# Performance work log

Measured on AMD Instinct MI355X. Metric: run time of the kernel, lower is better.

Reference implementation:

```python
import jax, jax.numpy as jnp
import numpy as np

N = 50000
E = 800000
NODE_IN, EDGE_IN, HID, OUT, L = 32, 16, 128, 128, 2


def _layer_norm(h, g, b, eps=1e-5):
    mu = jnp.mean(h, axis=-1, keepdims=True)
    var = jnp.var(h, axis=-1, keepdims=True)
    return (h - mu) * jax.lax.rsqrt(var + eps) * g + b


def setup_inputs() -> dict:
    key = jax.random.key(0)
    ks = jax.random.split(key, 20)
    s = lambda k, shape, fan: jax.random.normal(k, shape, jnp.float32) * (1.0 / np.sqrt(fan))
    return {
        "x": jax.random.normal(ks[0], (N, NODE_IN), jnp.float32),
        "edge_index": jax.random.randint(ks[1], (2, E), 0, N, jnp.int64),
        "edge_attr": jax.random.normal(ks[2], (E, EDGE_IN), jnp.float32),
        "enc_W": s(ks[3], (NODE_IN, HID), NODE_IN),
        "enc_b": jnp.zeros((HID,), jnp.float32),
        "enc_g": jnp.ones((HID,), jnp.float32),
        "enc_beta": jnp.zeros((HID,), jnp.float32),
        "msg_W1": s(ks[4], (L, 2 * HID + EDGE_IN, HID), 2 * HID + EDGE_IN),
        "msg_b1": jnp.zeros((L, HID), jnp.float32),
        "msg_W2": s(ks[5], (L, HID, HID), HID),
        "msg_b2": jnp.zeros((L, HID), jnp.float32),
        "upd_W1": s(ks[6], (L, 2 * HID, HID), 2 * HID),
        "upd_b1": jnp.zeros((L, HID), jnp.float32),
        "upd_W2": s(ks[7], (L, HID, HID), HID),
        "upd_b2": jnp.zeros((L, HID), jnp.float32),
        "ln_g": jnp.ones((L, HID), jnp.float32),
        "ln_beta": jnp.zeros((L, HID), jnp.float32),
        "head_W": s(ks[8], (HID, OUT), HID),
        "head_b": jnp.zeros((OUT,), jnp.float32),
    }


def reference(x, edge_index, edge_attr, enc_W, enc_b, enc_g, enc_beta,
              msg_W1, msg_b1, msg_W2, msg_b2, upd_W1, upd_b1, upd_W2, upd_b2,
              ln_g, ln_beta, head_W, head_b):
    src = edge_index[0]  # x_j (source)
    tgt = edge_index[1]  # x_i (target, aggregation index)
    n = x.shape[0]

    # node encoder: Linear -> ReLU -> LayerNorm
    h = jax.nn.relu(x @ enc_W + enc_b)
    h = _layer_norm(h, enc_g, enc_beta)

    # per-edge incoming-degree for mean aggregation (isolated nodes -> 0)
    cnt = jax.ops.segment_sum(jnp.ones((tgt.shape[0],), h.dtype), tgt, num_segments=n)
    denom = jnp.maximum(cnt, 1.0)[:, None]

    for l in range(L):
        x_i = h[tgt]                                 # [E, HID]
        x_j = h[src]                                 # [E, HID]
        msg_in = jnp.concatenate([x_i, x_j, edge_attr], axis=-1)  # [E, 2H+Ed]
        m = jax.nn.relu(msg_in @ msg_W1[l] + msg_b1[l]) @ msg_W2[l] + msg_b2[l]
        aggr = jax.ops.segment_sum(m, tgt, num_segments=n) / denom  # mean
        upd_in = jnp.concatenate([h, aggr], axis=-1)
        out = jax.nn.relu(upd_in @ upd_W1[l] + upd_b1[l]) @ upd_W2[l] + upd_b2[l]
        h = _layer_norm(h + out, ln_g[l], ln_beta[l])

    return h @ head_W + head_b
```

## Files before the change

### kernel.cpp

```cpp
#include <hip/hip_runtime.h>
#include <hip/hip_bf16.h>
#include <stdint.h>

#define N_NODES 50000
#define N_EDGES 800000
#define NL 2

#define KS2 136
#define KSU 264
#define ESTR 132

typedef __bf16 bf16x8 __attribute__((ext_vector_type(8)));
typedef float f32x4 __attribute__((ext_vector_type(4)));

__device__ __forceinline__ f32x4 mfma_bf16(uint4 a, uint4 b, f32x4 c) {
    return __builtin_amdgcn_mfma_f32_16x16x32_bf16(
        __builtin_bit_cast(bf16x8, a), __builtin_bit_cast(bf16x8, b), c, 0, 0, 0);
}

__device__ __forceinline__ unsigned short f2b(float f) {
    union { float f; unsigned u; } v; v.f = f;
    unsigned r = v.u + 0x7FFFu + ((v.u >> 16) & 1u);
    return (unsigned short)(r >> 16);
}

__device__ __forceinline__ float b2f(unsigned short u) {
    union { unsigned u; float f; } v; v.u = ((unsigned)u) << 16; return v.f;
}
__device__ __forceinline__ float b2f_lo(unsigned u) {
    union { unsigned u; float f; } v; v.u = u << 16; return v.f;
}
__device__ __forceinline__ float b2f_hi(unsigned u) {
    union { unsigned u; float f; } v; v.u = u & 0xFFFF0000u; return v.f;
}

template<int KSTEPS, int BSTR>
__device__ __forceinline__ void gemm8(const unsigned short* aLane,
                                      const unsigned short* bLane, f32x4 acc[8]) {
#pragma unroll
    for (int kc = 0; kc < KSTEPS; kc++) {
        uint4 a = *(const uint4*)(aLane + kc * 32);
#pragma unroll
        for (int ct = 0; ct < 8; ct++) {
            uint4 b = *(const uint4*)(bLane + (size_t)ct * 16 * BSTR + kc * 32);
            acc[ct] = mfma_bf16(a, b, acc[ct]);
        }
    }
}

template<int KSTEPS, int ASTR, int BSTR>
__device__ __forceinline__ void gemm_2x4(const unsigned short* aLane,
                                         const unsigned short* bLane,
                                         f32x4 acc[4][2]) {
#pragma unroll
    for (int kc = 0; kc < KSTEPS; kc++) {
        uint4 b0 = *(const uint4*)(bLane + kc * 32);
        uint4 b1 = *(const uint4*)(bLane + (size_t)16 * BSTR + kc * 32);
#pragma unroll
        for (int rt = 0; rt < 4; rt++) {
            uint4 a = *(const uint4*)(aLane + (size_t)rt * 16 * ASTR + kc * 32);
            acc[rt][0] = mfma_bf16(a, b0, acc[rt][0]);
            acc[rt][1] = mfma_bf16(a, b1, acc[rt][1]);
        }
    }
}

__global__ void prep_kernel(const float* __restrict__ mW1,
                            const float* __restrict__ uW1, const float* __restrict__ uW2,
                            const float* __restrict__ hW,
                            unsigned short* __restrict__ wab, unsigned short* __restrict__ w1cp,
                            unsigned short* __restrict__ u1t, unsigned short* __restrict__ u2t,
                            unsigned short* __restrict__ ht) {
    int i = blockIdx.x * 256 + threadIdx.x;
    const int SA = NL * 256 * 136;
    const int SC = NL * 128 * 32;
    const int SU = NL * 128 * KSU;
    const int S3 = NL * 128 * KS2;
    const int S4 = 128 * KS2;
    if (i < SA) {
        int l = i / (256 * 136), r = i % (256 * 136), j = r / 136, k = r % 136;
        float v = 0.f;
        if (k < 128)
            v = (j < 128) ? mW1[((size_t)l * 272 + k) * 128 + j]
                          : mW1[((size_t)l * 272 + 128 + k) * 128 + (j - 128)];
        wab[i] = f2b(v);
        return;
    }
    i -= SA;
    if (i < SC) {
        int l = i / (128 * 32), r = i % (128 * 32), j = r / 32, k = r % 32;
        w1cp[i] = (k < 16) ? f2b(mW1[((size_t)l * 272 + 256 + k) * 128 + j]) : (unsigned short)0;
        return;
    }
    i -= SC;
    if (i < SU) {
        int l = i / (128 * KSU), r = i % (128 * KSU), n = r / KSU, k = r % KSU;
        if (k < 128)       u1t[i] = f2b(uW1[((size_t)l * 256 + k) * 128 + n]);
        else if (k >= 256) u1t[i] = 0;
        return;
    }
    i -= SU;
    if (i < S3) {
        int l = i / (128 * KS2), r = i % (128 * KS2), n = r / KS2, k = r % KS2;
        u2t[i] = (k < 128) ? f2b(uW2[((size_t)l * 128 + k) * 128 + n]) : (unsigned short)0;
        return;
    }
    i -= S3;
    if (i < S4) {
        int n = i / KS2, k = i % KS2;
        ht[i] = (k < 128) ? f2b(hW[(size_t)k * 128 + n]) : (unsigned short)0;
    }
}

__global__ void prep2_kernel(const float* __restrict__ mW2, const float* __restrict__ uW1,
                             unsigned short* __restrict__ u1t) {
    __shared__ float w2row[128];
    const int l = blockIdx.x >> 7, j = blockIdx.x & 127;
    const int n = threadIdx.x;
    w2row[n] = mW2[((size_t)l * 128 + j) * 128 + n];
    __syncthreads();
    float s = 0.f;
#pragma unroll 8
    for (int c = 0; c < 128; c++)
        s += w2row[c] * uW1[((size_t)l * 256 + 128 + c) * 128 + n];
    u1t[(size_t)l * 128 * KSU + (size_t)n * KSU + 128 + j] = f2b(s);
}

__global__ void prep3_kernel(const float* __restrict__ mb2, const float* __restrict__ uW1,
                             float* __restrict__ bfold) {
    const int l = blockIdx.x;
    const int n = threadIdx.x;
    float s = 0.f;
#pragma unroll 8
    for (int c = 0; c < 128; c++)
        s += mb2[l * 128 + c] * uW1[((size_t)l * 256 + 128 + c) * 128 + n];
    bfold[l * 128 + n] = s;
}

__global__ __launch_bounds__(256) void enc_kernel(
        const float* __restrict__ x, const float* __restrict__ W,
        const float* __restrict__ b, const float* __restrict__ g, const float* __restrict__ bet,
        float* __restrict__ h, unsigned short* __restrict__ hb) {
    __shared__ float sx[64];
    __shared__ float redS[4], redSS[4];
    const int t = threadIdx.x;
    const int nb = blockIdx.x * 2;
    if (t < 64) sx[t] = x[(size_t)nb * 32 + t];
    __syncthreads();
    const int half = t >> 7, j = t & 127;
    const int node = nb + half;
    float acc = b[j];
#pragma unroll
    for (int k = 0; k < 32; k++) acc += sx[half * 32 + k] * W[k * 128 + j];
    float v = fmaxf(acc, 0.f);
    float s = v, ss = v * v;
#pragma unroll
    for (int d = 32; d > 0; d >>= 1) { s += __shfl_down(s, d); ss += __shfl_down(ss, d); }
    const int wv = t >> 6;
    if ((t & 63) == 0) { redS[wv] = s; redSS[wv] = ss; }
    __syncthreads();
    float S = redS[half * 2] + redS[half * 2 + 1];
    float SS = redSS[half * 2] + redSS[half * 2 + 1];
    float mu = S * (1.f / 128.f);
    float var = SS * (1.f / 128.f) - mu * mu;
    float rs = rsqrtf(var + 1e-5f);
    float o = (v - mu) * rs * g[j] + bet[j];
    h[(size_t)node * 128 + j] = o;
    hb[(size_t)node * 128 + j] = f2b(o);
}

__global__ void hist_kernel(const int* __restrict__ tgt, int* __restrict__ hist) {
    int i = blockIdx.x * 256 + threadIdx.x;
    atomicAdd(hist + tgt[i], 1);
}

__global__ void scan1_kernel(const int* __restrict__ hist, int* __restrict__ incl,
                             int* __restrict__ blksum) {
    __shared__ int buf[256];
    const int t = threadIdx.x;
    const int i = blockIdx.x * 256 + t;
    int v = (i < N_NODES) ? hist[i] : 0;
    buf[t] = v; __syncthreads();
#pragma unroll
    for (int d = 1; d < 256; d <<= 1) {
        int x = (t >= d) ? buf[t - d] : 0;
        __syncthreads();
        buf[t] += x;
        __syncthreads();
    }
    if (i < N_NODES) incl[i] = buf[t];
    if (t == 255) blksum[blockIdx.x] = buf[255];
}

__global__ void scan2_kernel(int* __restrict__ blksum, int nblk) {
    __shared__ int buf[256];
    const int t = threadIdx.x;
    int v = (t < nblk) ? blksum[t] : 0;
    buf[t] = v; __syncthreads();
#pragma unroll
    for (int d = 1; d < 256; d <<= 1) {
        int x = (t >= d) ? buf[t - d] : 0;
        __syncthreads();
        buf[t] += x;
        __syncthreads();
    }
    if (t < nblk) blksum[t] = buf[t];
}

__global__ void scan3_kernel(int* __restrict__ incl, const int* __restrict__ blksum,
                             const int* __restrict__ hist) {
    const int i = blockIdx.x * 256 + threadIdx.x;
    if (i >= N_NODES) return;
    const int b = blockIdx.x;
    const int base = (b > 0) ? blksum[b - 1] : 0;
    incl[i] = incl[i] + base - hist[i];
}

__global__ void scatterp_kernel(const int* __restrict__ src, const int* __restrict__ tgt,
                                int* __restrict__ cursor, uint2* __restrict__ permst) {
    const int e = blockIdx.x * 256 + threadIdx.x;
    const int tg = tgt[e];
    const int p = atomicAdd(cursor + tg, 1);
    permst[p] = make_uint2((unsigned)e, ((unsigned)src[e] << 16) | (unsigned)tg);
}

__global__ __launch_bounds__(256) void gather_kernel(
        const uint2* __restrict__ permst, const float* __restrict__ ea,
        unsigned int* __restrict__ sST, unsigned short* __restrict__ eabS) {
    const int p = blockIdx.x * 256 + threadIdx.x;
    const uint2 v = permst[p];
    sST[p] = v.y;
    const float4* s = (const float4*)(ea + (size_t)v.x * 16);
    ushort4* d = (ushort4*)(eabS + (size_t)p * 16);
#pragma unroll
    for (int i = 0; i < 4; i++) {
        float4 f = s[i];
        d[i] = make_ushort4(f2b(f.x), f2b(f.y), f2b(f.z), f2b(f.w));
    }
}

__global__ __launch_bounds__(256, 4) void node_kernel(
        const unsigned short* __restrict__ hb, const unsigned short* __restrict__ wab,
        const float* __restrict__ b1,
        unsigned short* __restrict__ Tb, unsigned short* __restrict__ Sb) {
    __shared__ __align__(16) unsigned short As[64 * KS2];
    const int t = threadIdx.x;
    const int n0 = blockIdx.x * 64;
    {
        const int m = t >> 2, q = t & 3;
        const int node = n0 + m;
        uint4* dst = (uint4*)(As + m * KS2);
        if (node < N_NODES) {
            const uint4* s = (const uint4*)(hb + (size_t)node * 128);
#pragma unroll
            for (int i = 0; i < 4; i++) dst[q * 4 + i] = s[q * 4 + i];
        } else {
            uint4 z{0, 0, 0, 0};
            for (int i = q; i < 16; i += 4) dst[i] = z;
        }
    }
    __syncthreads();

    const int wv = t >> 6, lane = t & 63, lr = lane & 15, lq = lane >> 4;
    const int cb = wv * 64;
    const f32x4 z4 = {0.f, 0.f, 0.f, 0.f};
    f32x4 acc[4][4];
#pragma unroll
    for (int i = 0; i < 4; i++)
#pragma unroll
        for (int j = 0; j < 4; j++) acc[i][j] = z4;

    const unsigned short* aL = As + lr * KS2 + lq * 8;
    const unsigned short* bL = wab + (size_t)(cb + lr) * KS2 + lq * 8;
#pragma unroll
    for (int kc = 0; kc < 4; kc++) {
        uint4 bA = *(const uint4*)(bL + kc * 32);
        uint4 bB = *(const uint4*)(bL + (size_t)16 * KS2 + kc * 32);
        uint4 bC = *(const uint4*)(bL + (size_t)32 * KS2 + kc * 32);
        uint4 bD = *(const uint4*)(bL + (size_t)48 * KS2 + kc * 32);
#pragma unroll
        for (int rt = 0; rt < 4; rt++) {
            uint4 a = *(const uint4*)(aL + (size_t)rt * 16 * KS2 + kc * 32);
            acc[rt][0] = mfma_bf16(a, bA, acc[rt][0]);
            acc[rt][1] = mfma_bf16(a, bB, acc[rt][1]);
            acc[rt][2] = mfma_bf16(a, bC, acc[rt][2]);
            acc[rt][3] = mfma_bf16(a, bD, acc[rt][3]);
        }
    }
#pragma unroll
    for (int ct = 0; ct < 4; ct++) {
        const int j = cb + ct * 16 + lr;
        const float bias = (j < 128) ? b1[j] : 0.f;
#pragma unroll
        for (int rt = 0; rt < 4; rt++) {
#pragma unroll
            for (int r = 0; r < 4; r++) {
                const int node = n0 + rt * 16 + lq * 4 + r;
                if (node < N_NODES) {
                    const float v = acc[rt][ct][r] + bias;
                    if (j < 128) Tb[(size_t)node * 128 + j] = f2b(v);
                    else         Sb[(size_t)node * 128 + (j - 128)] = f2b(v);
                }
            }
        }
    }
}

__global__ __launch_bounds__(256, 8) void edge_kernel(
        const unsigned short* __restrict__ eabS,
        const unsigned int* __restrict__ sST,
        const unsigned short* __restrict__ w1cp,
        const unsigned short* __restrict__ Tb, const unsigned short* __restrict__ Sb,
        float* __restrict__ aggr) {
    __shared__ __align__(16) float Es[32 * ESTR];
    __shared__ int sT[64];
    __shared__ int sS[64];

    const int t = threadIdx.x;
    const int e0 = blockIdx.x * 64;
    if (t < 64) {
        const unsigned v = sST[e0 + t];
        sT[t] = (int)(v & 0xFFFFu);
        sS[t] = (int)(v >> 16);
    }
    __syncthreads();

    const int wv = t >> 6, lane = t & 63, lr = lane & 15, lq = lane >> 4;
    const int rtw = (wv >> 1) * 16;
    const int cbw = (wv & 1) * 64;
    const int m = t & 31, c8b = t >> 5;
    const f32x4 z4 = {0.f, 0.f, 0.f, 0.f};

    unsigned long long bmask;
    {
        const int l = t & 63;
        const int a = sT[l];
        const int b = (l > 0) ? sT[l - 1] : a;
        bmask = __ballot(a != b);
    }

    uint4 t0a, t0b, s0a, s0b;
    {
        const unsigned short* Tr = Tb + (size_t)sT[m] * 128;
        const unsigned short* Sr = Sb + (size_t)sS[m] * 128;
        t0a = *(const uint4*)(Tr + c8b * 8);
        t0b = *(const uint4*)(Tr + c8b * 8 + 64);
        s0a = *(const uint4*)(Sr + c8b * 8);
        s0b = *(const uint4*)(Sr + c8b * 8 + 64);
    }

    float s = 0.f;
    bool first = true;

    {
        uint4 a = {0, 0, 0, 0};
        if (lq < 2)
            a = *(const uint4*)(eabS + (size_t)(e0 + rtw + lr) * 16 + lq * 8);
        f32x4 acc[4];
#pragma unroll
        for (int ct = 0; ct < 4; ct++) {
            uint4 b = *(const uint4*)(w1cp + (cbw + ct * 16 + lr) * 32 + lq * 8);
            acc[ct] = mfma_bf16(a, b, z4);
        }
#pragma unroll
        for (int ct = 0; ct < 4; ct++) {
            const int col = cbw + ct * 16 + lr;
#pragma unroll
            for (int r = 0; r < 4; r++)
                Es[(rtw + lq * 4 + r) * ESTR + col] = acc[ct][r];
        }
    }
    __syncthreads();

    uint4 t1a, t1b, s1a, s1b;
    {
        float* Erow = Es + m * ESTR;
        float4* EA = (float4*)(Erow + c8b * 8);
        float4* EB = (float4*)(Erow + c8b * 8 + 64);
        float4 ea0 = EA[0], ea1 = EA[1];
        ea0.x = fmaxf(ea0.x + b2f_lo(t0a.x) + b2f_lo(s0a.x), 0.f);
        ea0.y = fmaxf(ea0.y + b2f_hi(t0a.x) + b2f_hi(s0a.x), 0.f);
        ea0.z = fmaxf(ea0.z + b2f_lo(t0a.y) + b2f_lo(s0a.y), 0.f);
        ea0.w = fmaxf(ea0.w + b2f_hi(t0a.y) + b2f_hi(s0a.y), 0.f);
        ea1.x = fmaxf(ea1.x + b2f_lo(t0a.z) + b2f_lo(s0a.z), 0.f);
        ea1.y = fmaxf(ea1.y + b2f_hi(t0a.z) + b2f_hi(s0a.z), 0.f);
        ea1.z = fmaxf(ea1.z + b2f_lo(t0a.w) + b2f_lo(s0a.w), 0.f);
        ea1.w = fmaxf(ea1.w + b2f_hi(t0a.w) + b2f_hi(s0a.w), 0.f);
        EA[0] = ea0; EA[1] = ea1;
        float4 eb0 = EB[0], eb1 = EB[1];
        eb0.x = fmaxf(eb0.x + b2f_lo(t0b.x) + b2f_lo(s0b.x), 0.f);
        eb0.y = fmaxf(eb0.y + b2f_hi(t0b.x) + b2f_hi(s0b.x), 0.f);
        eb0.z = fmaxf(eb0.z + b2f_lo(t0b.y) + b2f_lo(s0b.y), 0.f);
        eb0.w = fmaxf(eb0.w + b2f_hi(t0b.y) + b2f_hi(s0b.y), 0.f);
        eb1.x = fmaxf(eb1.x + b2f_lo(t0b.z) + b2f_lo(s0b.z), 0.f);
        eb1.y = fmaxf(eb1.y + b2f_hi(t0b.z) + b2f_hi(s0b.z), 0.f);
        eb1.z = fmaxf(eb1.z + b2f_lo(t0b.w) + b2f_lo(s0b.w), 0.f);
        eb1.w = fmaxf(eb1.w + b2f_hi(t0b.w) + b2f_hi(s0b.w), 0.f);
        EB[0] = eb0; EB[1] = eb1;

        const unsigned short* Tr = Tb + (size_t)sT[32 + m] * 128;
        const unsigned short* Sr = Sb + (size_t)sS[32 + m] * 128;
        t1a = *(const uint4*)(Tr + c8b * 8);
        t1b = *(const uint4*)(Tr + c8b * 8 + 64);
        s1a = *(const uint4*)(Sr + c8b * 8);
        s1b = *(const uint4*)(Sr + c8b * 8 + 64);
    }
    __syncthreads();

    if (t < 128) {
        const int c = t;
        const unsigned mh = (unsigned)bmask;
#pragma unroll
        for (int i8 = 0; i8 < 4; i8++) {
            float v[8];
#pragma unroll
            for (int j = 0; j < 8; j++) v[j] = Es[(i8 * 8 + j) * ESTR + c];
#pragma unroll
            for (int j = 0; j < 8; j++) {
                const int i = i8 * 8 + j;
                if (mh & (1u << i)) {
                    float* dst = aggr + (size_t)sT[i - 1] * 128 + c;
                    if (first) { atomicAdd(dst, s); first = false; }
                    else       { *dst = s; }
                    s = 0.f;
                }
                s += v[j];
            }
        }
    }
    __syncthreads();

    {
        uint4 a = {0, 0, 0, 0};
        if (lq < 2)
            a = *(const uint4*)(eabS + (size_t)(e0 + 32 + rtw + lr) * 16 + lq * 8);
        f32x4 acc[4];
#pragma unroll
        for (int ct = 0; ct < 4; ct++) {
            uint4 b = *(const uint4*)(w1cp + (cbw + ct * 16 + lr) * 32 + lq * 8);
            acc[ct] = mfma_bf16(a, b, z4);
        }
#pragma unroll
        for (int ct = 0; ct < 4; ct++) {
            const int col = cbw + ct * 16 + lr;
#pragma unroll
            for (int r = 0; r < 4; r++)
                Es[(rtw + lq * 4 + r) * ESTR + col] = acc[ct][r];
        }
    }
    __syncthreads();

    {
        float* Erow = Es + m * ESTR;
        float4* EA = (float4*)(Erow + c8b * 8);
        float4* EB = (float4*)(Erow + c8b * 8 + 64);
        float4 ea0 = EA[0], ea1 = EA[1];
        ea0.x = fmaxf(ea0.x + b2f_lo(t1a.x) + b2f_lo(s1a.x), 0.f);
        ea0.y = fmaxf(ea0.y + b2f_hi(t1a.x) + b2f_hi(s1a.x), 0.f);
        ea0.z = fmaxf(ea0.z + b2f_lo(t1a.y) + b2f_lo(s1a.y), 0.f);
        ea0.w = fmaxf(ea0.w + b2f_hi(t1a.y) + b2f_hi(s1a.y), 0.f);
        ea1.x = fmaxf(ea1.x + b2f_lo(t1a.z) + b2f_lo(s1a.z), 0.f);
        ea1.y = fmaxf(ea1.y + b2f_hi(t1a.z) + b2f_hi(s1a.z), 0.f);
        ea1.z = fmaxf(ea1.z + b2f_lo(t1a.w) + b2f_lo(s1a.w), 0.f);
        ea1.w = fmaxf(ea1.w + b2f_hi(t1a.w) + b2f_hi(s1a.w), 0.f);
        EA[0] = ea0; EA[1] = ea1;
        float4 eb0 = EB[0], eb1 = EB[1];
        eb0.x = fmaxf(eb0.x + b2f_lo(t1b.x) + b2f_lo(s1b.x), 0.f);
        eb0.y = fmaxf(eb0.y + b2f_hi(t1b.x) + b2f_hi(s1b.x), 0.f);
        eb0.z = fmaxf(eb0.z + b2f_lo(t1b.y) + b2f_lo(s1b.y), 0.f);
        eb0.w = fmaxf(eb0.w + b2f_hi(t1b.y) + b2f_hi(s1b.y), 0.f);
        eb1.x = fmaxf(eb1.x + b2f_lo(t1b.z) + b2f_lo(s1b.z), 0.f);
        eb1.y = fmaxf(eb1.y + b2f_hi(t1b.z) + b2f_hi(s1b.z), 0.f);
        eb1.z = fmaxf(eb1.z + b2f_lo(t1b.w) + b2f_lo(s1b.w), 0.f);
        eb1.w = fmaxf(eb1.w + b2f_hi(t1b.w) + b2f_hi(s1b.w), 0.f);
        EB[0] = eb0; EB[1] = eb1;
    }
    __syncthreads();

    if (t < 128) {
        const int c = t;
        const unsigned mh = (unsigned)(bmask >> 32);
#pragma unroll
        for (int i8 = 0; i8 < 4; i8++) {
            float v[8];
#pragma unroll
            for (int j = 0; j < 8; j++) v[j] = Es[(i8 * 8 + j) * ESTR + c];
#pragma unroll
            for (int j = 0; j < 8; j++) {
                const int i = i8 * 8 + j;
                if (mh & (1u << i)) {
                    float* dst = aggr + (size_t)sT[32 + i - 1] * 128 + c;
                    if (first) { atomicAdd(dst, s); first = false; }
                    else       { *dst = s; }
                    s = 0.f;
                }
                s += v[j];
            }
        }
        atomicAdd(aggr + (size_t)sT[63] * 128 + c, s);
    }
}

__global__ __launch_bounds__(256, 4) void upd_kernel(
        const unsigned short* __restrict__ hb_in, const float* __restrict__ h_in,
        const float* __restrict__ aggr, const int* __restrict__ hist,
        const unsigned short* __restrict__ u1t, const unsigned short* __restrict__ u2t,
        const float* __restrict__ b1, const float* __restrict__ bf,
        const float* __restrict__ b2,
        const float* __restrict__ g, const float* __restrict__ bet,
        float* __restrict__ h_out, unsigned short* __restrict__ hb_out,
        const unsigned short* __restrict__ ht, const float* __restrict__ hbias,
        float* __restrict__ out, const int fuse) {
    __shared__ __align__(16) char smemA[64 * KSU * 2];
    __shared__ float sF[64];
    unsigned short* As = (unsigned short*)smemA;
    float* LNb = (float*)smemA;

    const int t = threadIdx.x;
    const int n0 = blockIdx.x * 64;
    {
        const int m = t >> 2, q = t & 3;
        const int node = n0 + m;
        unsigned short* row = As + m * KSU;
        if (node < N_NODES) {
            const uint4* ph = (const uint4*)(hb_in + (size_t)node * 128);
            uint4* d0 = (uint4*)row;
#pragma unroll
            for (int i = 0; i < 4; i++) d0[q * 4 + i] = ph[q * 4 + i];
            const int cntv = hist[node];
            if (q == 0) sF[m] = (cntv > 0) ? 1.f : 0.f;
            const float rden = 1.0f / fmaxf((float)cntv, 1.0f);
            const float4* pa = (const float4*)(aggr + (size_t)node * 128 + q * 32);
            ushort4* d1 = (ushort4*)(row + 128 + q * 32);
#pragma unroll
            for (int i = 0; i < 8; i++) {
                float4 v = pa[i];
                d1[i] = make_ushort4(f2b(v.x * rden), f2b(v.y * rden),
                                     f2b(v.z * rden), f2b(v.w * rden));
            }
            if (q == 0) { uint4 z{0, 0, 0, 0}; ((uint4*)(row + 256))[0] = z; }
        } else {
            if (q == 0) sF[m] = 0.f;
            uint4 z{0, 0, 0, 0};
            uint4* d = (uint4*)row;
            for (int i = q; i < 33; i += 4) d[i] = z;
        }
    }
    __syncthreads();

    const int wv = t >> 6, lane = t & 63, lr = lane & 15, lq = lane >> 4;
    const int cb = wv * 32;
    const f32x4 z4 = {0.f, 0.f, 0.f, 0.f};

    f32x4 acc[4][2];
#pragma unroll
    for (int i = 0; i < 4; i++) { acc[i][0] = z4; acc[i][1] = z4; }
    gemm_2x4<8, KSU, KSU>(As + lr * KSU + lq * 8,
                          u1t + (size_t)(cb + lr) * KSU + lq * 8, acc);
    __syncthreads();

#pragma unroll
    for (int ct = 0; ct < 2; ct++) {
        const int col = cb + ct * 16 + lr;
        const float bv = b1[col];
        const float bfv = bf[col];
#pragma unroll
        for (int rt = 0; rt < 4; rt++) {
#pragma unroll
            for (int r = 0; r < 4; r++) {
                const int ml = rt * 16 + lq * 4 + r;
                float v = fmaxf(acc[rt][ct][r] + bv + sF[ml] * bfv, 0.f);
                As[ml * KSU + col] = f2b(v);
            }
        }
    }
    __syncthreads();

    f32x4 acc2[4][2];
#pragma unroll
    for (int i = 0; i < 4; i++) { acc2[i][0] = z4; acc2[i][1] = z4; }
    gemm_2x4<4, KSU, KS2>(As + lr * KSU + lq * 8,
                          u2t + (size_t)(cb + lr) * KS2 + lq * 8, acc2);
    __syncthreads();

#pragma unroll
    for (int ct = 0; ct < 2; ct++) {
        const int col = cb + ct * 16 + lr;
        const float bv = b2[col];
#pragma unroll
        for (int rt = 0; rt < 4; rt++) {
#pragma unroll
            for (int r = 0; r < 4; r++) {
                const int ml = rt * 16 + lq * 4 + r;
                const int node = n0 + ml;
                if (node < N_NODES)
                    LNb[ml * 132 + col] = acc2[rt][ct][r] + bv + h_in[(size_t)node * 128 + col];
            }
        }
    }
    __syncthreads();

    {
        const int r = t >> 2, c0 = (t & 3) * 32;
        const int node = n0 + r;
        const bool valid = (node < N_NODES);
        float vbuf[32];
        if (valid) {
            float s = 0.f, ss = 0.f;
#pragma unroll
            for (int i = 0; i < 32; i++) { float v = LNb[r * 132 + c0 + i]; s += v; ss += v * v; }
            s += __shfl_xor(s, 1); ss += __shfl_xor(ss, 1);
            s += __shfl_xor(s, 2); ss += __shfl_xor(ss, 2);
            const float mu = s * (1.0f / 128.0f);
            const float var = ss * (1.0f / 128.0f) - mu * mu;
            const float rs = rsqrtf(var + 1e-5f);
#pragma unroll
            for (int i = 0; i < 32; i++) {
                const int j = c0 + i;
                vbuf[i] = (LNb[r * 132 + j] - mu) * rs * g[j] + bet[j];
            }
            if (!fuse) {
#pragma unroll
                for (int i = 0; i < 32; i++) {
                    const int j = c0 + i;
                    h_out[(size_t)node * 128 + j] = vbuf[i];
                    hb_out[(size_t)node * 128 + j] = f2b(vbuf[i]);
                }
            }
        }
        if (fuse) {
            __syncthreads();
            unsigned short* Ah = (unsigned short*)smemA;
#pragma unroll
            for (int i = 0; i < 32; i++)
                Ah[r * KS2 + c0 + i] = valid ? f2b(vbuf[i]) : (unsigned short)0;
            __syncthreads();
            const int m0 = wv * 16;
            f32x4 hacc[8];
#pragma unroll
            for (int i = 0; i < 8; i++) hacc[i] = z4;
            gemm8<4, KS2>(Ah + (size_t)(m0 + lr) * KS2 + lq * 8,
                          ht + (size_t)lr * KS2 + lq * 8, hacc);
#pragma unroll
            for (int ct = 0; ct < 8; ct++) {
                const int col = ct * 16 + lr;
                const float bv = hbias[col];
#pragma unroll
                for (int r2 = 0; r2 < 4; r2++) {
                    const int node2 = n0 + m0 + lq * 4 + r2;
                    if (node2 < N_NODES) out[(size_t)node2 * 128 + col] = hacc[ct][r2] + bv;
                }
            }
        }
    }
}

extern "C" void kernel_launch(void* const* d_in, const int* in_sizes, int n_in,
                              void* d_out, int out_size, void* d_ws, size_t ws_size,
                              hipStream_t stream) {
    const float* x       = (const float*)d_in[0];
    const int*   ei      = (const int*)d_in[1];
    const float* ea      = (const float*)d_in[2];
    const float* encW    = (const float*)d_in[3];
    const float* encb    = (const float*)d_in[4];
    const float* encg    = (const float*)d_in[5];
    const float* encbeta = (const float*)d_in[6];
    const float* msgW1   = (const float*)d_in[7];
    const float* msgb1   = (const float*)d_in[8];
    const float* msgW2   = (const float*)d_in[9];
    const float* msgb2   = (const float*)d_in[10];
    const float* updW1   = (const float*)d_in[11];
    const float* updb1   = (const float*)d_in[12];
    const float* updW2   = (const float*)d_in[13];
    const float* updb2   = (const float*)d_in[14];
    const float* lng     = (const float*)d_in[15];
    const float* lnbeta  = (const float*)d_in[16];
    const float* headW   = (const float*)d_in[17];
    const float* headb   = (const float*)d_in[18];

    char* w = (char*)d_ws;
    size_t off = 0;
    auto nxt = [&](size_t bytes) -> void* {
        void* p = w + off;
        off = (off + bytes + 255) & ~(size_t)255;
        return p;
    };
    float*          h     = (float*)nxt((size_t)N_NODES * 128 * 4);
    unsigned short* hb    = (unsigned short*)nxt((size_t)N_NODES * 128 * 2);
    float*          aggr  = (float*)nxt((size_t)N_NODES * 128 * 4);
    unsigned short* Tb    = (unsigned short*)nxt((size_t)N_NODES * 128 * 2);
    unsigned short* Sb    = (unsigned short*)nxt((size_t)N_NODES * 128 * 2);
    unsigned short* eabS  = (unsigned short*)nxt((size_t)N_EDGES * 16 * 2);
    unsigned int*   sST   = (unsigned int*)nxt((size_t)N_EDGES * 4);
    int*            hist  = (int*)nxt((size_t)N_NODES * 4);
    int*            incl  = (int*)nxt((size_t)N_NODES * 4);
    int*            blksum= (int*)nxt(256 * 4);
    unsigned short* wab   = (unsigned short*)nxt((size_t)NL * 256 * 136 * 2);
    unsigned short* w1cp  = (unsigned short*)nxt((size_t)NL * 128 * 32 * 2);
    unsigned short* u1t   = (unsigned short*)nxt((size_t)NL * 128 * KSU * 2);
    unsigned short* u2t   = (unsigned short*)nxt((size_t)NL * 128 * KS2 * 2);
    unsigned short* ht    = (unsigned short*)nxt((size_t)128 * KS2 * 2);
    float*          bfold = (float*)nxt((size_t)NL * 128 * 4);

    uint2*          permst = (uint2*)aggr;

    const int NBLK = (N_NODES + 255) / 256;
    const int PREP_N = NL * 256 * 136 + NL * 128 * 32 + NL * 128 * KSU
                     + NL * 128 * KS2 + 128 * KS2;

    hipMemsetAsync(hist, 0, (size_t)N_NODES * 4, stream);
    prep_kernel<<<(PREP_N + 255) / 256, 256, 0, stream>>>(msgW1, updW1, updW2, headW,
                                                          wab, w1cp, u1t, u2t, ht);
    prep2_kernel<<<NL * 128, 128, 0, stream>>>(msgW2, updW1, u1t);
    prep3_kernel<<<NL, 128, 0, stream>>>(msgb2, updW1, bfold);
    enc_kernel<<<25000, 256, 0, stream>>>(x, encW, encb, encg, encbeta, h, hb);
    hist_kernel<<<3125, 256, 0, stream>>>(ei + N_EDGES, hist);
    scan1_kernel<<<NBLK, 256, 0, stream>>>(hist, incl, blksum);
    scan2_kernel<<<1, 256, 0, stream>>>(blksum, NBLK);
    scan3_kernel<<<NBLK, 256, 0, stream>>>(incl, blksum, hist);
    scatterp_kernel<<<3125, 256, 0, stream>>>(ei, ei + N_EDGES, incl, permst);
    gather_kernel<<<3125, 256, 0, stream>>>(permst, ea, sST, eabS);

    for (int l = 0; l < NL; l++) {
        node_kernel<<<782, 256, 0, stream>>>(hb, wab + (size_t)l * 256 * 136,
                                             msgb1 + l * 128, Tb, Sb);
        hipMemsetAsync(aggr, 0, (size_t)N_NODES * 128 * 4, stream);
        edge_kernel<<<12500, 256, 0, stream>>>(eabS, sST,
                                               w1cp + (size_t)l * 128 * 32,
                                               Tb, Sb, aggr);
        upd_kernel<<<782, 256, 0, stream>>>(hb, h, aggr, hist,
                                            u1t + (size_t)l * 128 * KSU,
                                            u2t + (size_t)l * 128 * KS2,
                                            updb1 + l * 128, bfold + l * 128,
                                            updb2 + l * 128,
                                            lng + l * 128, lnbeta + l * 128, h, hb,
                                            ht, headb, (float*)d_out,
                                            (l == NL - 1) ? 1 : 0);
    }
}
```

Before: 539.7 us.

## Fuse next-layer node projection into update kernel and drop fp32 hidden state

The update kernel now runs the next layer's node-side projection (Tb/Sb) straight from the layer-normed tile it already holds in shared memory, so the standalone node_kernel is launched only once, for layer 0. The fp32 copy of h is removed and the residual is read from the bf16 hb buffer, which cuts global traffic and one kernel launch per layer. In exchange the residual add loses precision (bf16 instead of fp32), and upd_kernel carries an extra GEMM epilogue that may raise register pressure.

New measurement: 519.8 us. 3.7% less time.

```diff
diff --git a/kernel.cpp b/kernel.cpp
--- a/kernel.cpp
+++ b/kernel.cpp
@@ -24,14 +24,14 @@
     return (unsigned short)(r >> 16);
 }
 
-__device__ __forceinline__ float b2f(unsigned short u) {
-    union { unsigned u; float f; } v; v.u = ((unsigned)u) << 16; return v.f;
-}
 __device__ __forceinline__ float b2f_lo(unsigned u) {
     union { unsigned u; float f; } v; v.u = u << 16; return v.f;
 }
 __device__ __forceinline__ float b2f_hi(unsigned u) {
     union { unsigned u; float f; } v; v.u = u & 0xFFFF0000u; return v.f;
+}
+__device__ __forceinline__ unsigned pk2(unsigned short a, unsigned short b) {
+    return (unsigned)a | ((unsigned)b << 16);
 }
 
 template<int KSTEPS, int BSTR>
@@ -140,7 +140,7 @@
 __global__ __launch_bounds__(256) void enc_kernel(
         const float* __restrict__ x, const float* __restrict__ W,
         const float* __restrict__ b, const float* __restrict__ g, const float* __restrict__ bet,
-        float* __restrict__ h, unsigned short* __restrict__ hb) {
+        unsigned short* __restrict__ hb) {
     __shared__ float sx[64];
     __shared__ float redS[4], redSS[4];
     const int t = threadIdx.x;
@@ -165,7 +165,6 @@
     float var = SS * (1.f / 128.f) - mu * mu;
     float rs = rsqrtf(var + 1e-5f);
     float o = (v - mu) * rs * g[j] + bet[j];
-    h[(size_t)node * 128 + j] = o;
     hb[(size_t)node * 128 + j] = f2b(o);
 }
 
@@ -502,15 +501,17 @@
 }
 
 __global__ __launch_bounds__(256, 4) void upd_kernel(
-        const unsigned short* __restrict__ hb_in, const float* __restrict__ h_in,
+        const unsigned short* __restrict__ hb_in,
         const float* __restrict__ aggr, const int* __restrict__ hist,
         const unsigned short* __restrict__ u1t, const unsigned short* __restrict__ u2t,
         const float* __restrict__ b1, const float* __restrict__ bf,
         const float* __restrict__ b2,
         const float* __restrict__ g, const float* __restrict__ bet,
-        float* __restrict__ h_out, unsigned short* __restrict__ hb_out,
+        unsigned short* __restrict__ hb_out,
+        const unsigned short* __restrict__ wabn, const float* __restrict__ b1n,
+        unsigned short* __restrict__ Tb, unsigned short* __restrict__ Sb,
         const unsigned short* __restrict__ ht, const float* __restrict__ hbias,
-        float* __restrict__ out, const int fuse) {
+        float* __restrict__ out, const int mode) {
     __shared__ __align__(16) char smemA[64 * KSU * 2];
     __shared__ float sF[64];
     unsigned short* As = (unsigned short*)smemA;
@@ -592,63 +593,123 @@
 #pragma unroll
             for (int r = 0; r < 4; r++) {
                 const int ml = rt * 16 + lq * 4 + r;
-                const int node = n0 + ml;
-                if (node < N_NODES)
-                    LNb[ml * 132 + col] = acc2[rt][ct][r] + bv + h_in[(size_t)node * 128 + col];
-            }
-        }
-    }
-    __syncthreads();
-
+                LNb[ml * 132 + col] = acc2[rt][ct][r] + bv;
+            }
+        }
+    }
+    __syncthreads();
+
+    const int r = t >> 2, c0 = (t & 3) * 32;
+    const int node = n0 + r;
+    const bool valid = (node < N_NODES);
+    float vbuf[32];
+    if (valid) {
+        const uint4* hq = (const uint4*)(hb_in + (size_t)node * 128 + c0);
+        float s = 0.f, ss = 0.f;
+#pragma unroll
+        for (int k8 = 0; k8 < 4; k8++) {
+            const uint4 u = hq[k8];
+            float hr[8] = {b2f_lo(u.x), b2f_hi(u.x), b2f_lo(u.y), b2f_hi(u.y),
+                           b2f_lo(u.z), b2f_hi(u.z), b2f_lo(u.w), b2f_hi(u.w)};
+#pragma unroll
+            for (int j = 0; j < 8; j++) {
+                const float v = LNb[r * 132 + c0 + k8 * 8 + j] + hr[j];
+                vbuf[k8 * 8 + j] = v;
+                s += v; ss += v * v;
+            }
+        }
+        s += __shfl_xor(s, 1); ss += __shfl_xor(ss, 1);
+        s += __shfl_xor(s, 2); ss += __shfl_xor(ss, 2);
+        const float mu = s * (1.0f / 128.0f);
+        const float var = ss * (1.0f / 128.0f) - mu * mu;
+        const float rs = rsqrtf(var + 1e-5f);
+#pragma unroll
+        for (int i = 0; i < 32; i++) {
+            const int j = c0 + i;
+            vbuf[i] = (vbuf[i] - mu) * rs * g[j] + bet[j];
+        }
+    }
+    __syncthreads();
+
+    unsigned short* Ah = (unsigned short*)smemA;
     {
-        const int r = t >> 2, c0 = (t & 3) * 32;
-        const int node = n0 + r;
-        const bool valid = (node < N_NODES);
-        float vbuf[32];
-        if (valid) {
-            float s = 0.f, ss = 0.f;
-#pragma unroll
-            for (int i = 0; i < 32; i++) { float v = LNb[r * 132 + c0 + i]; s += v; ss += v * v; }
-            s += __shfl_xor(s, 1); ss += __shfl_xor(ss, 1);
-            s += __shfl_xor(s, 2); ss += __shfl_xor(ss, 2);
-            const float mu = s * (1.0f / 128.0f);
-            const float var = ss * (1.0f / 128.0f) - mu * mu;
-            const float rs = rsqrtf(var + 1e-5f);
-#pragma unroll
-            for (int i = 0; i < 32; i++) {
-                const int j = c0 + i;
-                vbuf[i] = (LNb[r * 132 + j] - mu) * rs * g[j] + bet[j];
-            }
-            if (!fuse) {
-#pragma unroll
-                for (int i = 0; i < 32; i++) {
-                    const int j = c0 + i;
-                    h_out[(size_t)node * 128 + j] = vbuf[i];
-                    hb_out[(size_t)node * 128 + j] = f2b(vbuf[i]);
-                }
-            }
-        }
-        if (fuse) {
-            __syncthreads();
-            unsigned short* Ah = (unsigned short*)smemA;
-#pragma unroll
-            for (int i = 0; i < 32; i++)
-                Ah[r * KS2 + c0 + i] = valid ? f2b(vbuf[i]) : (unsigned short)0;
-            __syncthreads();
-            const int m0 = wv * 16;
-            f32x4 hacc[8];
-#pragma unroll
-            for (int i = 0; i < 8; i++) hacc[i] = z4;
-            gemm8<4, KS2>(Ah + (size_t)(m0 + lr) * KS2 + lq * 8,
-                          ht + (size_t)lr * KS2 + lq * 8, hacc);
-#pragma unroll
-            for (int ct = 0; ct < 8; ct++) {
-                const int col = ct * 16 + lr;
-                const float bv = hbias[col];
+        unsigned short hb16[32];
+#pragma unroll
+        for (int i = 0; i < 32; i++) hb16[i] = valid ? f2b(vbuf[i]) : (unsigned short)0;
+        uint4* arow = (uint4*)(Ah + (size_t)r * KS2 + c0);
+#pragma unroll
+        for (int k8 = 0; k8 < 4; k8++)
+            arow[k8] = make_uint4(pk2(hb16[k8 * 8 + 0], hb16[k8 * 8 + 1]),
+                                  pk2(hb16[k8 * 8 + 2], hb16[k8 * 8 + 3]),
+                                  pk2(hb16[k8 * 8 + 4], hb16[k8 * 8 + 5]),
+                                  pk2(hb16[k8 * 8 + 6], hb16[k8 * 8 + 7]));
+        if (mode == 2 && valid) {
+            uint4* drow = (uint4*)(hb_out + (size_t)node * 128 + c0);
+#pragma unroll
+            for (int k8 = 0; k8 < 4; k8++)
+                drow[k8] = make_uint4(pk2(hb16[k8 * 8 + 0], hb16[k8 * 8 + 1]),
+                                      pk2(hb16[k8 * 8 + 2], hb16[k8 * 8 + 3]),
+                                      pk2(hb16[k8 * 8 + 4], hb16[k8 * 8 + 5]),
+                                      pk2(hb16[k8 * 8 + 6], hb16[k8 * 8 + 7]));
+        }
+    }
+    __syncthreads();
+
+    if (mode == 1) {
+        const int m0 = wv * 16;
+        f32x4 hacc[8];
+#pragma unroll
+        for (int i = 0; i < 8; i++) hacc[i] = z4;
+        gemm8<4, KS2>(Ah + (size_t)(m0 + lr) * KS2 + lq * 8,
+                      ht + (size_t)lr * KS2 + lq * 8, hacc);
+#pragma unroll
+        for (int ct = 0; ct < 8; ct++) {
+            const int col = ct * 16 + lr;
+            const float bv = hbias[col];
+#pragma unroll
+            for (int r2 = 0; r2 < 4; r2++) {
+                const int node2 = n0 + m0 + lq * 4 + r2;
+                if (node2 < N_NODES) out[(size_t)node2 * 128 + col] = hacc[ct][r2] + bv;
+            }
+        }
+    } else {
+        const int cbn = wv * 64;
+        f32x4 accn[4][4];
+#pragma unroll
+        for (int i = 0; i < 4; i++)
+#pragma unroll
+            for (int j = 0; j < 4; j++) accn[i][j] = z4;
+        const unsigned short* aL = Ah + lr * KS2 + lq * 8;
+        const unsigned short* bL = wabn + (size_t)(cbn + lr) * KS2 + lq * 8;
+#pragma unroll
+        for (int kc = 0; kc < 4; kc++) {
+            uint4 bA = *(const uint4*)(bL + kc * 32);
+            uint4 bB = *(const uint4*)(bL + (size_t)16 * KS2 + kc * 32);
+            uint4 bC = *(const uint4*)(bL + (size_t)32 * KS2 + kc * 32);
+            uint4 bD = *(const uint4*)(bL + (size_t)48 * KS2 + kc * 32);
+#pragma unroll
+            for (int rt = 0; rt < 4; rt++) {
+                uint4 a = *(const uint4*)(aL + (size_t)rt * 16 * KS2 + kc * 32);
+                accn[rt][0] = mfma_bf16(a, bA, accn[rt][0]);
+                accn[rt][1] = mfma_bf16(a, bB, accn[rt][1]);
+                accn[rt][2] = mfma_bf16(a, bC, accn[rt][2]);
+                accn[rt][3] = mfma_bf16(a, bD, accn[rt][3]);
+            }
+        }
+#pragma unroll
+        for (int ct = 0; ct < 4; ct++) {
+            const int j = cbn + ct * 16 + lr;
+            const float bias = (j < 128) ? b1n[j] : 0.f;
+#pragma unroll
+            for (int rt = 0; rt < 4; rt++) {
 #pragma unroll
                 for (int r2 = 0; r2 < 4; r2++) {
-                    const int node2 = n0 + m0 + lq * 4 + r2;
-                    if (node2 < N_NODES) out[(size_t)node2 * 128 + col] = hacc[ct][r2] + bv;
+                    const int node2 = n0 + rt * 16 + lq * 4 + r2;
+                    if (node2 < N_NODES) {
+                        const float v = accn[rt][ct][r2] + bias;
+                        if (j < 128) Tb[(size_t)node2 * 128 + j] = f2b(v);
+                        else         Sb[(size_t)node2 * 128 + (j - 128)] = f2b(v);
+                    }
                 }
             }
         }
@@ -685,7 +746,6 @@
         off = (off + bytes + 255) & ~(size_t)255;
         return p;
     };
-    float*          h     = (float*)nxt((size_t)N_NODES * 128 * 4);
     unsigned short* hb    = (unsigned short*)nxt((size_t)N_NODES * 128 * 2);
     float*          aggr  = (float*)nxt((size_t)N_NODES * 128 * 4);
     unsigned short* Tb    = (unsigned short*)nxt((size_t)N_NODES * 128 * 2);
@@ -713,7 +773,7 @@
                                                           wab, w1cp, u1t, u2t, ht);
     prep2_kernel<<<NL * 128, 128, 0, stream>>>(msgW2, updW1, u1t);
     prep3_kernel<<<NL, 128, 0, stream>>>(msgb2, updW1, bfold);
-    enc_kernel<<<25000, 256, 0, stream>>>(x, encW, encb, encg, encbeta, h, hb);
+    enc_kernel<<<25000, 256, 0, stream>>>(x, encW, encb, encg, encbeta, hb);
     hist_kernel<<<3125, 256, 0, stream>>>(ei + N_EDGES, hist);
     scan1_kernel<<<NBLK, 256, 0, stream>>>(hist, incl, blksum);
     scan2_kernel<<<1, 256, 0, stream>>>(blksum, NBLK);
@@ -721,20 +781,24 @@
     scatterp_kernel<<<3125, 256, 0, stream>>>(ei, ei + N_EDGES, incl, permst);
     gather_kernel<<<3125, 256, 0, stream>>>(permst, ea, sST, eabS);
 
+    node_kernel<<<782, 256, 0, stream>>>(hb, wab, msgb1, Tb, Sb);
+
     for (int l = 0; l < NL; l++) {
-        node_kernel<<<782, 256, 0, stream>>>(hb, wab + (size_t)l * 256 * 136,
-                                             msgb1 + l * 128, Tb, Sb);
         hipMemsetAsync(aggr, 0, (size_t)N_NODES * 128 * 4, stream);
         edge_kernel<<<12500, 256, 0, stream>>>(eabS, sST,
                                                w1cp + (size_t)l * 128 * 32,
                                                Tb, Sb, aggr);
-        upd_kernel<<<782, 256, 0, stream>>>(hb, h, aggr, hist,
+        upd_kernel<<<782, 256, 0, stream>>>(hb, aggr, hist,
                                             u1t + (size_t)l * 128 * KSU,
                                             u2t + (size_t)l * 128 * KS2,
                                             updb1 + l * 128, bfold + l * 128,
                                             updb2 + l * 128,
-                                            lng + l * 128, lnbeta + l * 128, h, hb,
+                                            lng + l * 128, lnbeta + l * 128,
+                                            hb,
+                                            wab + (size_t)(l + 1 < NL ? l + 1 : 0) * 256 * 136,
+                                            msgb1 + (l + 1 < NL ? l + 1 : 0) * 128,
+                                            Tb, Sb,
                                             ht, headb, (float*)d_out,
-                                            (l == NL - 1) ? 1 : 0);
-    }
-}
+                                            (l == NL - 1) ? 1 : 2);
+    }
+}
```
